# Kernel optimization log

Measured on AMD Instinct MI355X. Metric: run time of the kernel, lower is better.

Reference implementation:

```python
import jax, jax.numpy as jnp
import numpy as np

N_NODES = {'movie': 50000, 'director': 10000, 'actor': 25000}
# relation name -> (src_type, dst_type, num_edges)
RELS = {'md': ('movie', 'director', 150000),
        'dm': ('director', 'movie', 150000),
        'ma': ('movie', 'actor', 300000),
        'am': ('actor', 'movie', 300000)}
F_IN, HID, HEADS, OUT = 1024, 256, 8, 4
HD = HID // HEADS  # 32 per-head dim


def setup_inputs() -> dict:
    key = jax.random.key(0)
    kit = iter(jax.random.split(key, 128))
    def nrm(shape, s):
        return jax.random.normal(next(kit), shape, jnp.float32) * s
    inp = {}
    for t, n in N_NODES.items():
        inp['x_' + t] = nrm((n, F_IN), 1.0)
    for rn, (st, dt, e) in RELS.items():
        inp['e_' + rn + '_src'] = jax.random.randint(next(kit), (e,), 0, N_NODES[st], dtype=jnp.int32)
        inp['e_' + rn + '_dst'] = jax.random.randint(next(kit), (e,), 0, N_NODES[dt], dtype=jnp.int32)
        inp['a_' + rn] = nrm((HEADS, HD, HD), 0.05)   # per-relation attention matrix
        inp['m_' + rn] = nrm((HEADS, HD, HD), 0.05)   # per-relation message matrix
        inp['p_' + rn] = jnp.ones((HEADS,), jnp.float32)  # relation priority
    for t in N_NODES:
        inp['W_in_' + t] = nrm((F_IN, HID), 0.02)
        inp['b_in_' + t] = jnp.zeros((HID,), jnp.float32)
        for nm in ('k', 'q', 'v'):
            inp['W' + nm + '_' + t] = nrm((HID, HID), 0.05)
            inp['b' + nm + '_' + t] = jnp.zeros((HID,), jnp.float32)
        inp['Wa_' + t] = nrm((HID, HID), 0.05)
        inp['ba_' + t] = jnp.zeros((HID,), jnp.float32)
        inp['skip_' + t] = jnp.array(1.0, jnp.float32)
    inp['W_out'] = nrm((HID, OUT), 0.05)
    inp['b_out'] = jnp.zeros((OUT,), jnp.float32)
    return inp


def _forward(p):
    # per-node-type input projection (the HGT.lin_dict step)
    h = {t: p['x_' + t] @ p['W_in_' + t] + p['b_in_' + t] for t in N_NODES}
    # per-type K/Q/V projections, reshaped to [N, H, D]
    def proj(nm):
        return {t: (h[t] @ p['W' + nm + '_' + t] + p['b' + nm + '_' + t]).reshape(-1, HEADS, HD)
                for t in N_NODES}
    k, q, v = proj('k'), proj('q'), proj('v')
    scale = 1.0 / np.sqrt(HD)
    # per-edge-type: gather, relation-transform, score
    buf = {t: [] for t in N_NODES}
    for rn, (st, dt, _) in RELS.items():
        si, di = p['e_' + rn + '_src'], p['e_' + rn + '_dst']
        ke = jnp.einsum('ehd,hdf->ehf', k[st][si], p['a_' + rn])  # [E,H,D]
        ve = jnp.einsum('ehd,hdf->ehf', v[st][si], p['m_' + rn])  # [E,H,D]
        al = (q[dt][di] * ke).sum(-1) * (p['p_' + rn] * scale)    # [E,H]
        buf[dt].append((di, al, ve))
    # destination-grouped segment softmax + scatter aggregation
    out = {}
    for t, n in N_NODES.items():
        di = jnp.concatenate([b[0] for b in buf[t]])
        al = jnp.concatenate([b[1] for b in buf[t]])
        ve = jnp.concatenate([b[2] for b in buf[t]])
        amax = jax.ops.segment_max(al, di, num_segments=n)        # [N,H]
        amax = jnp.where(jnp.isfinite(amax), amax, 0.0)
        ex = jnp.exp(al - amax[di])
        den = jax.ops.segment_sum(ex, di, num_segments=n)[di]
        w = ex / jnp.where(den > 0, den, 1.0)                     # [E,H]
        agg = jax.ops.segment_sum(w[:, :, None] * ve, di, num_segments=n).reshape(n, HID)
        o = jax.nn.gelu(agg @ p['Wa_' + t] + p['ba_' + t])
        beta = jax.nn.sigmoid(p['skip_' + t])                     # gated skip connection
        out[t] = beta * o + (1.0 - beta) * h[t]
    # final classifier on movie nodes
    return out['movie'] @ p['W_out'] + p['b_out']


def reference(x_movie, x_director, x_actor, e_md_src, e_md_dst, a_md, m_md, p_md, e_dm_src, e_dm_dst, a_dm, m_dm, p_dm, e_ma_src, e_ma_dst, a_ma, m_ma, p_ma, e_am_src, e_am_dst, a_am, m_am, p_am, W_in_movie, b_in_movie, Wk_movie, bk_movie, Wq_movie, bq_movie, Wv_movie, bv_movie, Wa_movie, ba_movie, skip_movie, W_in_director, b_in_director, Wk_director, bk_director, Wq_director, bq_director, Wv_director, bv_director, Wa_director, ba_director, skip_director, W_in_actor, b_in_actor, Wk_actor, bk_actor, Wq_actor, bq_actor, Wv_actor, bv_actor, Wa_actor, ba_actor, skip_actor, W_out, b_out):
    p = dict(locals())
    return _forward(p)
```

## Files before the change

kernel.cpp:

```cpp
#include <hip/hip_runtime.h>
#include <math.h>

#define NM 50000
#define ND 10000
#define NA 25000
#define E_DM 150000
#define E_AM 300000
#define E_TOT (E_DM + E_AM)
#define HID 256
#define HEADS 8
#define HD 32
#define FIN 1024
#define SCALE 0.17677669529663687f

typedef __attribute__((ext_vector_type(8))) short short8;
typedef __attribute__((ext_vector_type(4))) float f32x4;

typedef __attribute__((address_space(1))) const unsigned char gas_u8;
typedef __attribute__((address_space(3))) unsigned char las_u8;

__device__ __forceinline__ void gload16(const void* g, void* l) {
    gas_u8* gp = (gas_u8*)(unsigned long long)(uintptr_t)g;
    las_u8* lp = (las_u8*)(unsigned int)(uintptr_t)l;
    __builtin_amdgcn_global_load_lds((const __attribute__((address_space(1))) void*)gp,
                                     (__attribute__((address_space(3))) void*)lp, 16, 0, 0);
}

__device__ __forceinline__ unsigned int pk_bf16(float x, float y) {
    unsigned int a = __float_as_uint(x), b = __float_as_uint(y);
    a += 0x7FFFu + ((a >> 16) & 1u);
    b += 0x7FFFu + ((b >> 16) & 1u);
    return (a >> 16) | (b & 0xFFFF0000u);
}
__device__ __forceinline__ unsigned short to_bf16(float x) {
    unsigned int a = __float_as_uint(x);
    a += 0x7FFFu + ((a >> 16) & 1u);
    return (unsigned short)(a >> 16);
}
__device__ __forceinline__ float bf2f(unsigned short u) {
    return __uint_as_float(((unsigned int)u) << 16);
}

struct F4 { const float* W[4]; const float* b[4]; const float* a[4]; float* Wf[4]; float* bf[4]; };
__global__ void fold_w4(F4 f4) {
    int di = blockIdx.y;
    const float* W = f4.W[di]; const float* b = f4.b[di]; const float* a = f4.a[di];
    float* Wf = f4.Wf[di]; float* bf = f4.bf[di];
    int c = threadIdx.x;
    int h = c >> 5, f = c & 31;
    int r = blockIdx.x;
    float acc = 0.f;
    if (r < HID) {
        #pragma unroll
        for (int d = 0; d < HD; ++d)
            acc += W[r * HID + h * HD + d] * a[(h * HD + d) * HD + f];
        Wf[r * HID + c] = acc;
    } else {
        #pragma unroll
        for (int d = 0; d < HD; ++d)
            acc += b[h * HD + d] * a[(h * HD + d) * HD + f];
        bf[c] = acc;
    }
}

struct PDesc { const float* W; unsigned short* out; int K; int b0; };
struct PMulti { PDesc d[9]; int nd; };
__global__ void wt_pack(PMulti pm) {
    int bid = blockIdx.x; int di = 0;
    #pragma unroll
    for (int i = 1; i < 9; ++i) if (i < pm.nd && bid >= pm.d[i].b0) di = i;
    PDesc p = pm.d[di];
    int kstep = bid - p.b0;
    int t = threadIdx.x;
    #pragma unroll
    for (int i = 0; i < 32; ++i) {
        int idx = i * 256 + t;
        int n0 = idx >> 9, r = idx & 511, lane = r >> 3, j = r & 7;
        int k = kstep * 32 + (lane >> 4) * 8 + j;
        int c = n0 * 16 + (lane & 15);
        p.out[(size_t)kstep * 8192 + idx] = to_bf16(p.W[(size_t)k * HID + c]);
    }
}

struct GDesc {
    const void* A; const unsigned short* Bt; const float* bias; void* C;
    const void* hskip; const float* gate;
    const unsigned short* Bt2; const float* bias2; void* C2;
    const unsigned short* Bt3; const float* bias3; void* C3;
    int M; int K; int epi; int obf; int abf; int cls; int b0;
};
struct GMulti { GDesc d[5]; int nd; };

#define GBM 64

__launch_bounds__(512, 6)
__global__ void gemm_mfma(GMulti mu) {
    __shared__ __align__(16) unsigned char smem[40960];
    unsigned short* sB0 = (unsigned short*)smem;
    unsigned short* sB1 = sB0 + 8192;
    unsigned short* sA0 = (unsigned short*)(smem + 32768);
    unsigned short* sA1 = sA0 + 2048;
    unsigned short* sHf = (unsigned short*)smem;
    float* arr = (float*)smem;

    int bid = blockIdx.x;
    int di = 0;
    #pragma unroll
    for (int i = 1; i < 5; ++i)
        if (i < mu.nd && bid >= mu.d[i].b0) di = i;
    GDesc g = mu.d[di];
    int bm = (bid - g.b0) * GBM;
    int M = g.M, K = g.K;

    int t = threadIdx.x;
    int lane = t & 63;
    int w = t >> 6;
    int wp = w >> 1;
    int ch = w & 1;
    int l16 = lane & 15;

    int slot = t >> 1;
    int ss_ = slot >> 6;
    int sl  = slot & 63;
    int arow_f = bm + ss_ * 16 + (sl & 15);
    int ak0    = (sl >> 4) * 8 + (t & 1) * 4;
    const float* Ap = nullptr;
    const unsigned short* Abp = nullptr;
    if (g.abf) {
        if (w < 4) {
            int r = bm + w * 16 + l16;
            Abp = (const unsigned short*)g.A + (size_t)min(r, M - 1) * K + ((lane >> 4) * 8);
        }
    } else {
        Ap = (const float*)g.A + (size_t)min(arow_f, M - 1) * K + ak0;
    }

    f32x4 acc[8];
    #pragma unroll
    for (int n = 0; n < 8; ++n) acc[n] = (f32x4)(0.f);

    int nk = K >> 5;
    {
        const unsigned short* gB = g.Bt;
        gload16(gB + w * 512 + lane * 8, sB0 + w * 512);
        gload16(gB + (w + 8) * 512 + lane * 8, sB0 + (w + 8) * 512);
        if (g.abf) {
            if (w < 4) gload16(Abp, sA0 + w * 512);
        } else {
            float4 f = *(const float4*)(Ap);
            uint2 pk = make_uint2(pk_bf16(f.x, f.y), pk_bf16(f.z, f.w));
            *(uint2*)&sA0[slot * 8 + (t & 1) * 4] = pk;
        }
    }
    __syncthreads();

    int cur = 0;
    for (int ks = 0; ks < nk; ++ks) {
        unsigned short* sBc = cur ? sB1 : sB0;
        unsigned short* sAc = cur ? sA1 : sA0;
        unsigned short* dB  = cur ? sB0 : sB1;
        unsigned short* dA  = cur ? sA0 : sA1;
        bool pf = (ks + 1 < nk);
        float4 f;
        if (pf) {
            const unsigned short* gB = g.Bt + (size_t)(ks + 1) * 8192;
            gload16(gB + w * 512 + lane * 8, dB + w * 512);
            gload16(gB + (w + 8) * 512 + lane * 8, dB + (w + 8) * 512);
            if (g.abf) {
                if (w < 4) gload16(Abp + (ks + 1) * 32, dA + w * 512);
            } else {
                f = *(const float4*)(Ap + (ks + 1) * 32);
            }
        }
        short8 af = *(const short8*)&sAc[(wp * 64 + lane) * 8];
        short8 bfr[8];
        #pragma unroll
        for (int n = 0; n < 8; ++n)
            bfr[n] = *(const short8*)&sBc[((ch * 8 + n) * 64 + lane) * 8];
        #pragma unroll
        for (int n = 0; n < 8; ++n)
            acc[n] = __builtin_amdgcn_mfma_f32_16x16x32_bf16(af, bfr[n], acc[n], 0, 0, 0);
        if (pf && !g.abf) {
            uint2 pk = make_uint2(pk_bf16(f.x, f.y), pk_bf16(f.z, f.w));
            *(uint2*)&dA[slot * 8 + (t & 1) * 4] = pk;
        }
        __syncthreads();
        cur ^= 1;
    }

    float beta = 0.f;
    if (g.epi) beta = 1.f / (1.f + expf(-g.gate[0]));
    int r0 = bm + wp * 16 + ((lane >> 4) << 2);

    float pcl[4][4];
    if (g.cls) {
        #pragma unroll
        for (int j = 0; j < 4; ++j)
            #pragma unroll
            for (int c = 0; c < 4; ++c) pcl[j][c] = 0.f;
    }

    #pragma unroll
    for (int n = 0; n < 8; ++n) {
        int col = ch * 128 + n * 16 + l16;
        float4 wv;
        if (g.cls) wv = *(const float4*)(g.bias2 + col * 4);
        #pragma unroll
        for (int j = 0; j < 4; ++j) {
            int grow = r0 + j;
            float v = acc[n][j] + g.bias[col];
            if (g.epi) {
                float x = v;
                float gl = 0.5f * x * (1.f + tanhf(0.7978845608028654f * (x + 0.044715f * x * x * x)));
                float hv = bf2f(((const unsigned short*)g.hskip)[(size_t)min(grow, M - 1) * HID + col]);
                v = beta * gl + (1.f - beta) * hv;
            }
            if (g.cls) {
                pcl[j][0] += v * wv.x; pcl[j][1] += v * wv.y;
                pcl[j][2] += v * wv.z; pcl[j][3] += v * wv.w;
            } else {
                int ks2 = ch * 4 + (n >> 1);
                int gg = ((n & 1) << 1) | ((lane & 15) >> 3);
                int l = ((lane >> 4) << 2) + j + (gg << 4);
                sHf[(((ks2 * 4) + wp) * 64 + l) * 8 + (lane & 7)] = to_bf16(v);
                if (g.C && grow < M)
                    ((unsigned short*)g.C)[(size_t)grow * HID + col] = to_bf16(v);
            }
        }
    }

    if (g.cls) {
        #pragma unroll
        for (int s = 1; s < 16; s <<= 1) {
            #pragma unroll
            for (int j = 0; j < 4; ++j)
                #pragma unroll
                for (int c = 0; c < 4; ++c)
                    pcl[j][c] += __shfl_xor(pcl[j][c], s);
        }
        if (l16 == 0) {
            int rb = wp * 16 + ((lane >> 4) << 2);
            #pragma unroll
            for (int j = 0; j < 4; ++j)
                #pragma unroll
                for (int c = 0; c < 4; ++c)
                    arr[((ch * 64) + rb + j) * 4 + c] = pcl[j][c];
        }
        __syncthreads();
        if (t < 256) {
            int row = t >> 2, c = t & 3;
            int grow = bm + row;
            if (grow < M) {
                float s = arr[(0 * 64 + row) * 4 + c] + arr[(1 * 64 + row) * 4 + c] + g.bias3[c];
                ((float*)g.C2)[(size_t)grow * 4 + c] = s;
            }
        }
    } else if (g.Bt2) {
        __syncthreads();
        #pragma unroll 1
        for (int o = 0; o < 2; ++o) {
            const unsigned short* B2 = o ? g.Bt3 : g.Bt2;
            if (!B2) break;
            const float* bias2 = o ? g.bias3 : g.bias2;
            unsigned short* C2 = (unsigned short*)(o ? g.C3 : g.C2);
            f32x4 acc2[8];
            #pragma unroll
            for (int n = 0; n < 8; ++n) acc2[n] = (f32x4)(0.f);
            #pragma unroll 1
            for (int ks = 0; ks < 8; ++ks) {
                short8 af2 = *(const short8*)&sHf[(((ks * 4) + wp) * 64 + lane) * 8];
                #pragma unroll
                for (int n = 0; n < 8; ++n) {
                    short8 b2 = *(const short8*)(B2 + (size_t)ks * 8192 +
                                                 (size_t)(((ch * 8) + n) * 64 + lane) * 8);
                    acc2[n] = __builtin_amdgcn_mfma_f32_16x16x32_bf16(af2, b2, acc2[n], 0, 0, 0);
                }
            }
            #pragma unroll
            for (int n = 0; n < 8; ++n) {
                int col = ch * 128 + n * 16 + l16;
                #pragma unroll
                for (int j = 0; j < 4; ++j) {
                    int grow = r0 + j;
                    if (grow < M)
                        C2[(size_t)grow * HID + col] = to_bf16(acc2[n][j] + bias2[col]);
                }
            }
        }
    }
}

__global__ void hist_deg(const int* __restrict__ dA, const int* __restrict__ dB,
                         int* __restrict__ deg) {
    int i = blockIdx.x * 256 + threadIdx.x;
    if (i < E_DM) atomicAdd(&deg[dA[i]], 1);
    else if (i < E_TOT) atomicAdd(&deg[dB[i - E_DM]], 1);
}

__global__ void scan_pass1(const int* __restrict__ deg, int* __restrict__ bsum) {
    __shared__ int s[256];
    int b = blockIdx.x, t = threadIdx.x;
    int i = b * 256 + t;
    int v = (i < NM) ? deg[i] : 0;
    s[t] = v; __syncthreads();
    for (int off = 128; off > 0; off >>= 1) {
        if (t < off) s[t] += s[t + off];
        __syncthreads();
    }
    if (t == 0) bsum[b] = s[0];
}

__global__ void scan_pass2(const int* __restrict__ bsum, int* __restrict__ boff, int nb) {
    __shared__ int s[256];
    int t = threadIdx.x;
    int v = (t < nb) ? bsum[t] : 0;
    s[t] = v; __syncthreads();
    for (int off = 1; off < 256; off <<= 1) {
        int x = (t >= off) ? s[t - off] : 0;
        __syncthreads();
        s[t] += x;
        __syncthreads();
    }
    if (t < nb) boff[t] = s[t] - v;
}

__global__ void scan_pass3(const int* __restrict__ deg, const int* __restrict__ boff,
                           int* __restrict__ rowptr, int* __restrict__ cursor) {
    __shared__ int s[256];
    int b = blockIdx.x, t = threadIdx.x, i = b * 256 + t;
    int v = (i < NM) ? deg[i] : 0;
    s[t] = v; __syncthreads();
    for (int off = 1; off < 256; off <<= 1) {
        int x = (t >= off) ? s[t - off] : 0;
        __syncthreads();
        s[t] += x;
        __syncthreads();
    }
    int excl = s[t] - v + boff[b];
    if (i < NM) { rowptr[i] = excl; cursor[i] = excl; }
    if (i == 0) rowptr[NM] = E_TOT;
}

__global__ void fill_adj(const int* __restrict__ sA, const int* __restrict__ dA,
                         const int* __restrict__ sB, const int* __restrict__ dB,
                         int* __restrict__ cursor, int* __restrict__ adj) {
    int i = blockIdx.x * 256 + threadIdx.x;
    int d, entry;
    if (i < E_DM)      { d = dA[i];        entry = sA[i]; }
    else if (i < E_TOT){ int j = i - E_DM; d = dB[j]; entry = (sB[j] + ND) | (1 << 16); }
    else return;
    int pos = atomicAdd(&cursor[d], 1);
    adj[pos] = entry;
}

__launch_bounds__(256)
__global__ void agg_fused(const int* __restrict__ rowptr, const int* __restrict__ adj,
                          const unsigned short* __restrict__ q, const unsigned short* __restrict__ kt_all,
                          const unsigned short* __restrict__ vt_all,
                          const float* __restrict__ p_dm, const float* __restrict__ p_am,
                          unsigned short* __restrict__ agg) {
    int d = blockIdx.x * 4 + (threadIdx.x >> 6);
    if (d >= NM) return;
    int lane = threadIdx.x & 63;
    int h = lane >> 3;
    int start = rowptr[d], end = rowptr[d + 1];
    uint2 qu = *(const uint2*)(q + (size_t)d * HID + lane * 4);
    float q0 = __uint_as_float(qu.x << 16), q1 = __uint_as_float(qu.x & 0xFFFF0000u);
    float q2 = __uint_as_float(qu.y << 16), q3 = __uint_as_float(qu.y & 0xFFFF0000u);
    float pr0 = p_dm[h] * SCALE, pr1 = p_am[h] * SCALE;
    float m = -INFINITY, den = 0.f, a0 = 0.f, a1 = 0.f, a2 = 0.f, a3 = 0.f;
    for (int i = start; i < end; ++i) {
        int e = adj[i];
        int sr = e & 0xFFFF;
        uint2 ku = *(const uint2*)(kt_all + (size_t)sr * HID + lane * 4);
        float k0 = __uint_as_float(ku.x << 16), k1 = __uint_as_float(ku.x & 0xFFFF0000u);
        float k2 = __uint_as_float(ku.y << 16), k3 = __uint_as_float(ku.y & 0xFFFF0000u);
        float prod = q0 * k0 + q1 * k1 + q2 * k2 + q3 * k3;
        prod += __shfl_xor(prod, 1);
        prod += __shfl_xor(prod, 2);
        prod += __shfl_xor(prod, 4);
        float a = prod * ((e >> 16) ? pr1 : pr0);
        float mn = fmaxf(m, a);
        float c  = __expf(m - mn);
        float ex = __expf(a - mn);
        uint2 vu = *(const uint2*)(vt_all + (size_t)sr * HID + lane * 4);
        float v0 = __uint_as_float(vu.x << 16), v1 = __uint_as_float(vu.x & 0xFFFF0000u);
        float v2 = __uint_as_float(vu.y << 16), v3 = __uint_as_float(vu.y & 0xFFFF0000u);
        den = den * c + ex;
        a0 = a0 * c + ex * v0; a1 = a1 * c + ex * v1;
        a2 = a2 * c + ex * v2; a3 = a3 * c + ex * v3;
        m = mn;
    }
    float inv = (end > start) ? 1.f / den : 0.f;
    *(uint2*)(agg + (size_t)d * HID + lane * 4) =
        make_uint2(pk_bf16(a0 * inv, a1 * inv), pk_bf16(a2 * inv, a3 * inv));
}

extern "C" void kernel_launch(void* const* d_in, const int* in_sizes, int n_in,
                              void* d_out, int out_size, void* d_ws, size_t ws_size,
                              hipStream_t stream) {
    (void)in_sizes; (void)n_in; (void)out_size; (void)ws_size;
    const float* x_movie    = (const float*)d_in[0];
    const float* x_director = (const float*)d_in[1];
    const float* x_actor    = (const float*)d_in[2];
    const int*   e_dm_src = (const int*)d_in[8];
    const int*   e_dm_dst = (const int*)d_in[9];
    const float* a_dm     = (const float*)d_in[10];
    const float* m_dm     = (const float*)d_in[11];
    const float* p_dm     = (const float*)d_in[12];
    const int*   e_am_src = (const int*)d_in[18];
    const int*   e_am_dst = (const int*)d_in[19];
    const float* a_am     = (const float*)d_in[20];
    const float* m_am     = (const float*)d_in[21];
    const float* p_am     = (const float*)d_in[22];
    const float* W_in_m = (const float*)d_in[23];
    const float* b_in_m = (const float*)d_in[24];
    const float* Wq_m   = (const float*)d_in[27];
    const float* bq_m   = (const float*)d_in[28];
    const float* Wa_m   = (const float*)d_in[31];
    const float* ba_m   = (const float*)d_in[32];
    const float* skip_m = (const float*)d_in[33];
    const float* W_in_d = (const float*)d_in[34];
    const float* b_in_d = (const float*)d_in[35];
    const float* Wk_d   = (const float*)d_in[36];
    const float* bk_d   = (const float*)d_in[37];
    const float* Wv_d   = (const float*)d_in[40];
    const float* bv_d   = (const float*)d_in[41];
    const float* W_in_a = (const float*)d_in[45];
    const float* b_in_a = (const float*)d_in[46];
    const float* Wk_a   = (const float*)d_in[47];
    const float* bk_a   = (const float*)d_in[48];
    const float* Wv_a   = (const float*)d_in[51];
    const float* bv_a   = (const float*)d_in[52];
    const float* W_out  = (const float*)d_in[56];
    const float* b_out  = (const float*)d_in[57];

    char* base = (char*)d_ws;
    size_t off = 0;
    auto alloc = [&](size_t bytes) -> void* {
        void* p = base + off;
        off = (off + bytes + 255) & ~(size_t)255;
        return p;
    };
    unsigned short* h_m = (unsigned short*)alloc((size_t)NM * HID * 2);
    unsigned short* q_m = (unsigned short*)alloc((size_t)NM * HID * 2);
    unsigned short* agg = (unsigned short*)alloc((size_t)NM * HID * 2);
    unsigned short* kt_all = (unsigned short*)alloc((size_t)(ND + NA) * HID * 2);
    unsigned short* vt_all = (unsigned short*)alloc((size_t)(ND + NA) * HID * 2);
    float* Wf     = (float*)alloc(4 * (size_t)HID * HID * 4);
    float* bf     = (float*)alloc(4 * (size_t)HID * 4);
    int* deg      = (int*)alloc(NM * 4);
    int* rowptr   = (int*)alloc((NM + 1) * 4);
    int* cursor   = (int*)alloc(NM * 4);
    int* bsum     = (int*)alloc(256 * 4);
    int* boff     = (int*)alloc(256 * 4);
    int* adj      = (int*)alloc((size_t)E_TOT * 4);
    unsigned short* Bt_in_m = (unsigned short*)alloc((size_t)256 * 1024 * 2);
    unsigned short* Bt_in_d = (unsigned short*)alloc((size_t)256 * 1024 * 2);
    unsigned short* Bt_in_a = (unsigned short*)alloc((size_t)256 * 1024 * 2);
    unsigned short* Bt_q_m  = (unsigned short*)alloc((size_t)256 * 256 * 2);
    unsigned short* Bt_k_dm = (unsigned short*)alloc((size_t)256 * 256 * 2);
    unsigned short* Bt_v_dm = (unsigned short*)alloc((size_t)256 * 256 * 2);
    unsigned short* Bt_k_am = (unsigned short*)alloc((size_t)256 * 256 * 2);
    unsigned short* Bt_v_am = (unsigned short*)alloc((size_t)256 * 256 * 2);
    unsigned short* Bt_a_m  = (unsigned short*)alloc((size_t)256 * 256 * 2);

    unsigned short* kt_dm = kt_all;
    unsigned short* kt_am = kt_all + (size_t)ND * HID;
    unsigned short* vt_dm = vt_all;
    unsigned short* vt_am = vt_all + (size_t)ND * HID;

    float* Wf_k_dm = Wf + 0 * HID * HID;  float* bf_k_dm = bf + 0 * HID;
    float* Wf_v_dm = Wf + 1 * HID * HID;  float* bf_v_dm = bf + 1 * HID;
    float* Wf_k_am = Wf + 2 * HID * HID;  float* bf_k_am = bf + 2 * HID;
    float* Wf_v_am = Wf + 3 * HID * HID;  float* bf_v_am = bf + 3 * HID;

    hipMemsetAsync(deg, 0, NM * sizeof(int), stream);
    hist_deg<<<(E_TOT + 255) / 256, 256, 0, stream>>>(e_dm_dst, e_am_dst, deg);
    int nb = (NM + 255) / 256;
    scan_pass1<<<nb, 256, 0, stream>>>(deg, bsum);
    scan_pass2<<<1, 256, 0, stream>>>(bsum, boff, nb);
    scan_pass3<<<nb, 256, 0, stream>>>(deg, boff, rowptr, cursor);
    fill_adj<<<(E_TOT + 255) / 256, 256, 0, stream>>>(e_dm_src, e_dm_dst, e_am_src, e_am_dst,
                                                      cursor, adj);

    {
        F4 f4{};
        f4.W[0] = Wk_d; f4.b[0] = bk_d; f4.a[0] = a_dm; f4.Wf[0] = Wf_k_dm; f4.bf[0] = bf_k_dm;
        f4.W[1] = Wv_d; f4.b[1] = bv_d; f4.a[1] = m_dm; f4.Wf[1] = Wf_v_dm; f4.bf[1] = bf_v_dm;
        f4.W[2] = Wk_a; f4.b[2] = bk_a; f4.a[2] = a_am; f4.Wf[2] = Wf_k_am; f4.bf[2] = bf_k_am;
        f4.W[3] = Wv_a; f4.b[3] = bv_a; f4.a[3] = m_am; f4.Wf[3] = Wf_v_am; f4.bf[3] = bf_v_am;
        fold_w4<<<dim3(257, 4), 256, 0, stream>>>(f4);
    }
    {
        PMulti pm{};
        pm.nd = 9;
        int b0 = 0;
        pm.d[0] = {W_in_m,  Bt_in_m, FIN, b0}; b0 += 32;
        pm.d[1] = {W_in_d,  Bt_in_d, FIN, b0}; b0 += 32;
        pm.d[2] = {W_in_a,  Bt_in_a, FIN, b0}; b0 += 32;
        pm.d[3] = {Wq_m,    Bt_q_m,  HID, b0}; b0 += 8;
        pm.d[4] = {Wf_k_dm, Bt_k_dm, HID, b0}; b0 += 8;
        pm.d[5] = {Wf_v_dm, Bt_v_dm, HID, b0}; b0 += 8;
        pm.d[6] = {Wf_k_am, Bt_k_am, HID, b0}; b0 += 8;
        pm.d[7] = {Wf_v_am, Bt_v_am, HID, b0}; b0 += 8;
        pm.d[8] = {Wa_m,    Bt_a_m,  HID, b0}; b0 += 8;
        wt_pack<<<b0, 256, 0, stream>>>(pm);
    }

    int bm_m = (NM + GBM - 1) / GBM;
    int bm_d = (ND + GBM - 1) / GBM;
    int bm_a = (NA + GBM - 1) / GBM;

    {
        GMulti mu{};
        mu.nd = 3;
        mu.d[0] = {x_movie, Bt_in_m, b_in_m, h_m, nullptr, nullptr,
                   Bt_q_m, bq_m, q_m, nullptr, nullptr, nullptr,
                   NM, FIN, 0, 1, 0, 0, 0};
        mu.d[1] = {x_director, Bt_in_d, b_in_d, nullptr, nullptr, nullptr,
                   Bt_k_dm, bf_k_dm, kt_dm, Bt_v_dm, bf_v_dm, vt_dm,
                   ND, FIN, 0, 1, 0, 0, bm_m};
        mu.d[2] = {x_actor, Bt_in_a, b_in_a, nullptr, nullptr, nullptr,
                   Bt_k_am, bf_k_am, kt_am, Bt_v_am, bf_v_am, vt_am,
                   NA, FIN, 0, 1, 0, 0, bm_m + bm_d};
        gemm_mfma<<<bm_m + bm_d + bm_a, 512, 0, stream>>>(mu);
    }

    agg_fused<<<(NM + 3) / 4, 256, 0, stream>>>(rowptr, adj, q_m, kt_all, vt_all, p_dm, p_am, agg);

    {
        GMulti mu{};
        mu.nd = 1;
        mu.d[0] = {agg, Bt_a_m, ba_m, nullptr, h_m, skip_m,
                   nullptr, W_out, d_out, nullptr, b_out, nullptr,
                   NM, HID, 1, 0, 1, 1, 0};
        gemm_mfma<<<bm_m, 512, 0, stream>>>(mu);
    }
}
```

Measured before the change: 361.2 us.

## Coalesce GEMM epilogue stores via LDS and software-pipeline fused second GEMM B loads

Splits the classifier epilogue into its own early-return branch. In the non-classifier path the bf16 tile is written to shared memory first and then copied out to C as 16-byte rows, replacing scattered 2-byte global stores. The fused K/Q/V follow-on GEMM now prefetches B fragments one k-step ahead in two halves, reuses the main accumulator registers, and fully unrolls the k loop. Launch bounds are raised to 8 blocks per SM to gain occupancy, which tightens the register budget and risks spills.

```diff
diff --git a/kernel.cpp b/kernel.cpp
--- a/kernel.cpp
+++ b/kernel.cpp
@@ -93,7 +93,7 @@
 
 #define GBM 64
 
-__launch_bounds__(512, 6)
+__launch_bounds__(512, 8)
 __global__ void gemm_mfma(GMulti mu) {
     __shared__ __align__(16) unsigned char smem[40960];
     unsigned short* sB0 = (unsigned short*)smem;
@@ -192,44 +192,30 @@
     if (g.epi) beta = 1.f / (1.f + expf(-g.gate[0]));
     int r0 = bm + wp * 16 + ((lane >> 4) << 2);
 
-    float pcl[4][4];
     if (g.cls) {
+        float pcl[4][4];
         #pragma unroll
         for (int j = 0; j < 4; ++j)
             #pragma unroll
             for (int c = 0; c < 4; ++c) pcl[j][c] = 0.f;
-    }
-
-    #pragma unroll
-    for (int n = 0; n < 8; ++n) {
-        int col = ch * 128 + n * 16 + l16;
-        float4 wv;
-        if (g.cls) wv = *(const float4*)(g.bias2 + col * 4);
-        #pragma unroll
-        for (int j = 0; j < 4; ++j) {
-            int grow = r0 + j;
-            float v = acc[n][j] + g.bias[col];
-            if (g.epi) {
-                float x = v;
-                float gl = 0.5f * x * (1.f + tanhf(0.7978845608028654f * (x + 0.044715f * x * x * x)));
-                float hv = bf2f(((const unsigned short*)g.hskip)[(size_t)min(grow, M - 1) * HID + col]);
-                v = beta * gl + (1.f - beta) * hv;
-            }
-            if (g.cls) {
+        #pragma unroll
+        for (int n = 0; n < 8; ++n) {
+            int col = ch * 128 + n * 16 + l16;
+            float4 wv = *(const float4*)(g.bias2 + col * 4);
+            #pragma unroll
+            for (int j = 0; j < 4; ++j) {
+                int grow = r0 + j;
+                float v = acc[n][j] + g.bias[col];
+                if (g.epi) {
+                    float x = v;
+                    float gl = 0.5f * x * (1.f + tanhf(0.7978845608028654f * (x + 0.044715f * x * x * x)));
+                    float hv = bf2f(((const unsigned short*)g.hskip)[(size_t)min(grow, M - 1) * HID + col]);
+                    v = beta * gl + (1.f - beta) * hv;
+                }
                 pcl[j][0] += v * wv.x; pcl[j][1] += v * wv.y;
                 pcl[j][2] += v * wv.z; pcl[j][3] += v * wv.w;
-            } else {
-                int ks2 = ch * 4 + (n >> 1);
-                int gg = ((n & 1) << 1) | ((lane & 15) >> 3);
-                int l = ((lane >> 4) << 2) + j + (gg << 4);
-                sHf[(((ks2 * 4) + wp) * 64 + l) * 8 + (lane & 7)] = to_bf16(v);
-                if (g.C && grow < M)
-                    ((unsigned short*)g.C)[(size_t)grow * HID + col] = to_bf16(v);
             }
         }
-    }
-
-    if (g.cls) {
         #pragma unroll
         for (int s = 1; s < 16; s <<= 1) {
             #pragma unroll
@@ -255,26 +241,76 @@
                 ((float*)g.C2)[(size_t)grow * 4 + c] = s;
             }
         }
-    } else if (g.Bt2) {
-        __syncthreads();
+        return;
+    }
+
+    #pragma unroll
+    for (int n = 0; n < 8; ++n) {
+        int col = ch * 128 + n * 16 + l16;
+        #pragma unroll
+        for (int j = 0; j < 4; ++j) {
+            float v = acc[n][j] + g.bias[col];
+            if (g.epi) {
+                int grow = r0 + j;
+                float x = v;
+                float gl = 0.5f * x * (1.f + tanhf(0.7978845608028654f * (x + 0.044715f * x * x * x)));
+                float hv = bf2f(((const unsigned short*)g.hskip)[(size_t)min(grow, M - 1) * HID + col]);
+                v = beta * gl + (1.f - beta) * hv;
+            }
+            int ks2 = ch * 4 + (n >> 1);
+            int gg = ((n & 1) << 1) | ((lane & 15) >> 3);
+            int l = ((lane >> 4) << 2) + j + (gg << 4);
+            sHf[(((ks2 * 4) + wp) * 64 + l) * 8 + (lane & 7)] = to_bf16(v);
+        }
+    }
+    __syncthreads();
+
+    if (g.C) {
+        #pragma unroll
+        for (int it = 0; it < 4; ++it) {
+            int c = t + it * 512;
+            int ks2 = c >> 8;
+            int wp_ = (c >> 6) & 3;
+            int l = c & 63;
+            int grow = bm + wp_ * 16 + (l & 15);
+            uint4 vv = *(const uint4*)&sHf[c * 8];
+            if (grow < M)
+                *(uint4*)((unsigned short*)g.C + (size_t)grow * HID + ks2 * 32 + (l >> 4) * 8) = vv;
+        }
+    }
+
+    if (g.Bt2) {
         #pragma unroll 1
         for (int o = 0; o < 2; ++o) {
             const unsigned short* B2 = o ? g.Bt3 : g.Bt2;
             if (!B2) break;
             const float* bias2 = o ? g.bias3 : g.bias2;
             unsigned short* C2 = (unsigned short*)(o ? g.C3 : g.C2);
-            f32x4 acc2[8];
-            #pragma unroll
-            for (int n = 0; n < 8; ++n) acc2[n] = (f32x4)(0.f);
-            #pragma unroll 1
+            #pragma unroll
+            for (int n = 0; n < 8; ++n) acc[n] = (f32x4)(0.f);
+            const unsigned short* Bw = B2 + (size_t)((ch * 8) * 64 + lane) * 8;
+            short8 p[4];
+            #pragma unroll
+            for (int i = 0; i < 4; ++i)
+                p[i] = *(const short8*)(Bw + (size_t)(i * 64) * 8);
+            #pragma unroll
             for (int ks = 0; ks < 8; ++ks) {
+                short8 qv[4];
+                #pragma unroll
+                for (int i = 0; i < 4; ++i)
+                    qv[i] = *(const short8*)(Bw + (size_t)ks * 8192 + (size_t)((4 + i) * 64) * 8);
                 short8 af2 = *(const short8*)&sHf[(((ks * 4) + wp) * 64 + lane) * 8];
                 #pragma unroll
-                for (int n = 0; n < 8; ++n) {
-                    short8 b2 = *(const short8*)(B2 + (size_t)ks * 8192 +
-                                                 (size_t)(((ch * 8) + n) * 64 + lane) * 8);
-                    acc2[n] = __builtin_amdgcn_mfma_f32_16x16x32_bf16(af2, b2, acc2[n], 0, 0, 0);
+                for (int i = 0; i < 4; ++i)
+                    acc[i] = __builtin_amdgcn_mfma_f32_16x16x32_bf16(af2, p[i], acc[i], 0, 0, 0);
+                if (ks < 7) {
+                    #pragma unroll
+                    for (int i = 0; i < 4; ++i)
+                        p[i] = *(const short8*)(Bw + (size_t)(ks + 1) * 8192 + (size_t)(i * 64) * 8);
                 }
+                #pragma unroll
+                for (int i = 0; i < 4; ++i)
+                    acc[4 + i] = __builtin_amdgcn_mfma_f32_16x16x32_bf16(af2, qv[i], acc[4 + i], 0, 0, 0);
             }
             #pragma unroll
             for (int n = 0; n < 8; ++n) {
@@ -283,7 +319,7 @@
                 for (int j = 0; j < 4; ++j) {
                     int grow = r0 + j;
                     if (grow < M)
-                        C2[(size_t)grow * HID + col] = to_bf16(acc2[n][j] + bias2[col]);
+                        C2[(size_t)grow * HID + col] = to_bf16(acc[n][j] + bias2[col]);
                 }
             }
         }
```

Measured after the change: 534.9 us. +48.1%, slower.
